# Kernel tuning notes

Hardware: AMD Instinct MI355X
Metric: run time of the kernel (lower is better)

The kernel has to match this reference:

```python
import jax, jax.numpy as jnp
import numpy as np

EPS = 1e-12  # matches torch F.normalize eps


def _l2_normalize(x, axis=-1):
    # torch.F.normalize: x / max(||x||, eps)
    n = jnp.sqrt(jnp.sum(x * x, axis=axis, keepdims=True))
    return x / jnp.maximum(n, EPS)


def setup_inputs() -> dict:
    N, n_classes, embed_dim = 32768, 1000, 1024
    key = jax.random.key(0)
    k_feat, k_lab, k_proto = jax.random.split(key, 3)

    features = jax.random.normal(k_feat, (N, embed_dim), dtype=jnp.float32)

    # one-hot float labels, as expected by `torch.matmul(labels, self.mean_class)`
    y = jax.random.randint(k_lab, (N,), 0, n_classes)
    labels = jax.nn.one_hot(y, n_classes, dtype=jnp.float32)

    # predefined prototypes: orthonormal rows (ortho_group.rvs equivalent via QR)
    g = jax.random.normal(k_proto, (embed_dim, embed_dim), dtype=jnp.float32)
    q, _ = jnp.linalg.qr(g)
    mean_class = q[:n_classes]  # [n_classes, embed_dim], orthonormal rows

    return {"features": features, "labels": labels, "mean_class": mean_class}


def reference(features, labels, mean_class):
    # features: [N, D]; labels: [N, C] one-hot; mean_class: [C, D]
    # (3-D feature mean-pooling branch not exercised: inputs are 2-D)
    proto_y = labels @ mean_class                 # [N, D]
    f = _l2_normalize(features, axis=1)
    p = _l2_normalize(proto_y, axis=1)
    # diag(f @ p.T) == rowwise dot product -> same math, O(N*D) not O(N^2*D)
    cos = jnp.einsum("nd,nd->n", f, p)            # [N]
    return jnp.mean(1.0 - cos)
```

## Files before the change

kernel.cpp:

```cpp
#include <hip/hip_runtime.h>

constexpr int N_CLASSES = 1000;
constexpr int EMBED     = 1024;

typedef float floatx4 __attribute__((ext_vector_type(4)));

__global__ __launch_bounds__(256) void class_scan_kernel(
    const float* __restrict__ labels,
    int* __restrict__ cls_buf)
{
    const int row = blockIdx.x;
    const int t   = threadIdx.x;
    if (t < N_CLASSES / 4) {
        const floatx4* lrow = (const floatx4*)(labels + (size_t)row * N_CLASSES);
        floatx4 v = __builtin_nontemporal_load(lrow + t);
        if (v.x != 0.f || v.y != 0.f || v.z != 0.f || v.w != 0.f) {
            int c = 4 * t;
            if      (v.y != 0.f) c += 1;
            else if (v.z != 0.f) c += 2;
            else if (v.w != 0.f) c += 3;
            cls_buf[row] = c;
        }
    }
}

__global__ __launch_bounds__(256) void angular_dots_kernel(
    const float* __restrict__ features,
    const float* __restrict__ mean_class,
    const int* __restrict__ cls_buf,
    float* __restrict__ partials,
    int n_rows)
{
    const int tid  = threadIdx.x;
    const int lane = tid & 63;
    const int wave = tid >> 6;
    const int row  = blockIdx.x * 4 + wave;

    float res = 0.0f;

    if (row < n_rows) {
        const int cls = __builtin_amdgcn_readfirstlane(cls_buf[row]);

        const floatx4* frow = (const floatx4*)(features + (size_t)row * EMBED);
        const floatx4* prow = (const floatx4*)(mean_class + (size_t)cls * EMBED);

        floatx4 f0 = __builtin_nontemporal_load(frow + lane);
        floatx4 f1 = __builtin_nontemporal_load(frow + lane + 64);
        floatx4 f2 = __builtin_nontemporal_load(frow + lane + 128);
        floatx4 f3 = __builtin_nontemporal_load(frow + lane + 192);
        floatx4 p0 = prow[lane];
        floatx4 p1 = prow[lane + 64];
        floatx4 p2 = prow[lane + 128];
        floatx4 p3 = prow[lane + 192];

        float ff = 0.f, pp = 0.f, fp = 0.f;
        #define DOT3(F, P) \
            ff += F.x*F.x + F.y*F.y + F.z*F.z + F.w*F.w; \
            pp += P.x*P.x + P.y*P.y + P.z*P.z + P.w*P.w; \
            fp += F.x*P.x + F.y*P.y + F.z*P.z + F.w*P.w;
        DOT3(f0, p0) DOT3(f1, p1) DOT3(f2, p2) DOT3(f3, p3)
        #undef DOT3

        #pragma unroll
        for (int msk = 1; msk < 64; msk <<= 1) {
            ff += __shfl_xor(ff, msk, 64);
            pp += __shfl_xor(pp, msk, 64);
            fp += __shfl_xor(fp, msk, 64);
        }
        const float denom = fmaxf(sqrtf(ff), 1e-12f) * fmaxf(sqrtf(pp), 1e-12f);
        res = 1.0f - fp / denom;
    }

    __shared__ float s_red[4];
    if (lane == 0) s_red[wave] = res;
    __syncthreads();
    if (tid == 0)
        partials[blockIdx.x] = s_red[0] + s_red[1] + s_red[2] + s_red[3];
}

__global__ __launch_bounds__(256) void reduce_partials_kernel(
    const float* __restrict__ partials, int num_partials,
    float* __restrict__ out, float inv_n)
{
    const int tid  = threadIdx.x;
    const int lane = tid & 63;
    const int wave = tid >> 6;
    __shared__ float s_red[4];

    float acc = 0.0f;
    for (int i = tid; i < num_partials; i += 256)
        acc += partials[i];
    #pragma unroll
    for (int msk = 1; msk < 64; msk <<= 1)
        acc += __shfl_xor(acc, msk, 64);
    if (lane == 0) s_red[wave] = acc;
    __syncthreads();
    if (tid == 0)
        out[0] = (s_red[0] + s_red[1] + s_red[2] + s_red[3]) * inv_n;
}

extern "C" void kernel_launch(void* const* d_in, const int* in_sizes, int n_in,
                              void* d_out, int out_size, void* d_ws, size_t ws_size,
                              hipStream_t stream) {
    const float* features   = (const float*)d_in[0];
    const float* labels     = (const float*)d_in[1];
    const float* mean_class = (const float*)d_in[2];
    float* out = (float*)d_out;

    const int n_rows = in_sizes[0] / EMBED;
    int* cls_buf    = (int*)d_ws;
    float* partials = (float*)d_ws + n_rows;

    const int dot_blocks = (n_rows + 3) / 4;

    class_scan_kernel<<<n_rows, 256, 0, stream>>>(labels, cls_buf);
    angular_dots_kernel<<<dot_blocks, 256, 0, stream>>>(
        features, mean_class, cls_buf, partials, n_rows);
    reduce_partials_kernel<<<1, 256, 0, stream>>>(
        partials, dot_blocks, out, 1.0f / (float)n_rows);
}
```

Baseline: 260.8 us.

## Fuse label class scan into dot kernel, process eight rows per block

```diff
diff --git a/kernel.cpp b/kernel.cpp
--- a/kernel.cpp
+++ b/kernel.cpp
@@ -2,76 +2,99 @@
 
 constexpr int N_CLASSES = 1000;
 constexpr int EMBED     = 1024;
+constexpr int ROWS_PER_BLOCK = 8;
 
 typedef float floatx4 __attribute__((ext_vector_type(4)));
 
-__global__ __launch_bounds__(256) void class_scan_kernel(
+__global__ __launch_bounds__(256) void angular_fused_kernel(
+    const float* __restrict__ features,
     const float* __restrict__ labels,
-    int* __restrict__ cls_buf)
-{
-    const int row = blockIdx.x;
-    const int t   = threadIdx.x;
-    if (t < N_CLASSES / 4) {
-        const floatx4* lrow = (const floatx4*)(labels + (size_t)row * N_CLASSES);
-        floatx4 v = __builtin_nontemporal_load(lrow + t);
-        if (v.x != 0.f || v.y != 0.f || v.z != 0.f || v.w != 0.f) {
-            int c = 4 * t;
-            if      (v.y != 0.f) c += 1;
-            else if (v.z != 0.f) c += 2;
-            else if (v.w != 0.f) c += 3;
-            cls_buf[row] = c;
-        }
-    }
-}
-
-__global__ __launch_bounds__(256) void angular_dots_kernel(
-    const float* __restrict__ features,
     const float* __restrict__ mean_class,
-    const int* __restrict__ cls_buf,
     float* __restrict__ partials,
     int n_rows)
 {
     const int tid  = threadIdx.x;
     const int lane = tid & 63;
     const int wave = tid >> 6;
-    const int row  = blockIdx.x * 4 + wave;
+    const int row0 = blockIdx.x * ROWS_PER_BLOCK;
 
-    float res = 0.0f;
+    __shared__ int   s_cls[ROWS_PER_BLOCK];
+    __shared__ float s_red[4];
 
-    if (row < n_rows) {
-        const int cls = __builtin_amdgcn_readfirstlane(cls_buf[row]);
-
-        const floatx4* frow = (const floatx4*)(features + (size_t)row * EMBED);
-        const floatx4* prow = (const floatx4*)(mean_class + (size_t)cls * EMBED);
-
-        floatx4 f0 = __builtin_nontemporal_load(frow + lane);
-        floatx4 f1 = __builtin_nontemporal_load(frow + lane + 64);
-        floatx4 f2 = __builtin_nontemporal_load(frow + lane + 128);
-        floatx4 f3 = __builtin_nontemporal_load(frow + lane + 192);
-        floatx4 p0 = prow[lane];
-        floatx4 p1 = prow[lane + 64];
-        floatx4 p2 = prow[lane + 128];
-        floatx4 p3 = prow[lane + 192];
-
-        float ff = 0.f, pp = 0.f, fp = 0.f;
-        #define DOT3(F, P) \
-            ff += F.x*F.x + F.y*F.y + F.z*F.z + F.w*F.w; \
-            pp += P.x*P.x + P.y*P.y + P.z*P.z + P.w*P.w; \
-            fp += F.x*P.x + F.y*P.y + F.z*P.z + F.w*P.w;
-        DOT3(f0, p0) DOT3(f1, p1) DOT3(f2, p2) DOT3(f3, p3)
-        #undef DOT3
-
+    if (tid < N_CLASSES / 4) {
         #pragma unroll
-        for (int msk = 1; msk < 64; msk <<= 1) {
-            ff += __shfl_xor(ff, msk, 64);
-            pp += __shfl_xor(pp, msk, 64);
-            fp += __shfl_xor(fp, msk, 64);
+        for (int r = 0; r < ROWS_PER_BLOCK; ++r) {
+            const int row = row0 + r;
+            if (row < n_rows) {
+                const floatx4* lrow = (const floatx4*)(labels + (size_t)row * N_CLASSES);
+                floatx4 v = __builtin_nontemporal_load(lrow + tid);
+                if (v.x != 0.f || v.y != 0.f || v.z != 0.f || v.w != 0.f) {
+                    int c = 4 * tid;
+                    if      (v.y != 0.f) c += 1;
+                    else if (v.z != 0.f) c += 2;
+                    else if (v.w != 0.f) c += 3;
+                    s_cls[r] = c;
+                }
+            }
         }
-        const float denom = fmaxf(sqrtf(ff), 1e-12f) * fmaxf(sqrtf(pp), 1e-12f);
-        res = 1.0f - fp / denom;
     }
 
-    __shared__ float s_red[4];
+    const int rA = row0 + 2 * wave;
+    const int rB = rA + 1;
+    const bool okA = rA < n_rows, okB = rB < n_rows;
+
+    const floatx4* fArow = (const floatx4*)(features + (size_t)(okA ? rA : 0) * EMBED);
+    const floatx4* fBrow = (const floatx4*)(features + (size_t)(okB ? rB : 0) * EMBED);
+    floatx4 a0 = __builtin_nontemporal_load(fArow + lane);
+    floatx4 a1 = __builtin_nontemporal_load(fArow + lane + 64);
+    floatx4 a2 = __builtin_nontemporal_load(fArow + lane + 128);
+    floatx4 a3 = __builtin_nontemporal_load(fArow + lane + 192);
+    floatx4 b0 = __builtin_nontemporal_load(fBrow + lane);
+    floatx4 b1 = __builtin_nontemporal_load(fBrow + lane + 64);
+    floatx4 b2 = __builtin_nontemporal_load(fBrow + lane + 128);
+    floatx4 b3 = __builtin_nontemporal_load(fBrow + lane + 192);
+
+    __syncthreads();
+
+    const int clsA = okA ? s_cls[2 * wave] : 0;
+    const int clsB = okB ? s_cls[2 * wave + 1] : 0;
+    const floatx4* pArow = (const floatx4*)(mean_class + (size_t)clsA * EMBED);
+    const floatx4* pBrow = (const floatx4*)(mean_class + (size_t)clsB * EMBED);
+    floatx4 pa0 = pArow[lane];
+    floatx4 pa1 = pArow[lane + 64];
+    floatx4 pa2 = pArow[lane + 128];
+    floatx4 pa3 = pArow[lane + 192];
+    floatx4 pb0 = pBrow[lane];
+    floatx4 pb1 = pBrow[lane + 64];
+    floatx4 pb2 = pBrow[lane + 128];
+    floatx4 pb3 = pBrow[lane + 192];
+
+    float ffA = 0.f, ppA = 0.f, fpA = 0.f;
+    float ffB = 0.f, ppB = 0.f, fpB = 0.f;
+    #define DOT3(FF, PP, FP, F, P) \
+        FF += F.x*F.x + F.y*F.y + F.z*F.z + F.w*F.w; \
+        PP += P.x*P.x + P.y*P.y + P.z*P.z + P.w*P.w; \
+        FP += F.x*P.x + F.y*P.y + F.z*P.z + F.w*P.w;
+    DOT3(ffA, ppA, fpA, a0, pa0) DOT3(ffA, ppA, fpA, a1, pa1)
+    DOT3(ffA, ppA, fpA, a2, pa2) DOT3(ffA, ppA, fpA, a3, pa3)
+    DOT3(ffB, ppB, fpB, b0, pb0) DOT3(ffB, ppB, fpB, b1, pb1)
+    DOT3(ffB, ppB, fpB, b2, pb2) DOT3(ffB, ppB, fpB, b3, pb3)
+    #undef DOT3
+
+    #pragma unroll
+    for (int msk = 1; msk < 64; msk <<= 1) {
+        ffA += __shfl_xor(ffA, msk, 64);
+        ppA += __shfl_xor(ppA, msk, 64);
+        fpA += __shfl_xor(fpA, msk, 64);
+        ffB += __shfl_xor(ffB, msk, 64);
+        ppB += __shfl_xor(ppB, msk, 64);
+        fpB += __shfl_xor(fpB, msk, 64);
+    }
+
+    float res = 0.f;
+    if (okA) res += 1.0f - fpA / (fmaxf(sqrtf(ffA), 1e-12f) * fmaxf(sqrtf(ppA), 1e-12f));
+    if (okB) res += 1.0f - fpB / (fmaxf(sqrtf(ffB), 1e-12f) * fmaxf(sqrtf(ppB), 1e-12f));
+
     if (lane == 0) s_red[wave] = res;
     __syncthreads();
     if (tid == 0)
@@ -106,16 +129,13 @@
     const float* labels     = (const float*)d_in[1];
     const float* mean_class = (const float*)d_in[2];
     float* out = (float*)d_out;
+    float* partials = (float*)d_ws;
 
     const int n_rows = in_sizes[0] / EMBED;
-    int* cls_buf    = (int*)d_ws;
-    float* partials = (float*)d_ws + n_rows;
+    const int num_blocks = (n_rows + ROWS_PER_BLOCK - 1) / ROWS_PER_BLOCK;
 
-    const int dot_blocks = (n_rows + 3) / 4;
-
-    class_scan_kernel<<<n_rows, 256, 0, stream>>>(labels, cls_buf);
-    angular_dots_kernel<<<dot_blocks, 256, 0, stream>>>(
-        features, mean_class, cls_buf, partials, n_rows);
+    angular_fused_kernel<<<num_blocks, 256, 0, stream>>>(
+        features, labels, mean_class, partials, n_rows);
     reduce_partials_kernel<<<1, 256, 0, stream>>>(
-        partials, dot_blocks, out, 1.0f / (float)n_rows);
+        partials, num_blocks, out, 1.0f / (float)n_rows);
 }
```

Result: no change. 258.3 us (-0.9%).
